# Optimization experiments

Measured on AMD Instinct MI355X. Metric: run time of the kernel, lower is better.

The kernel has to match this reference:

```python
import jax, jax.numpy as jnp
import numpy as np

EMB = 1024
NUM_HEADS = 16


def setup_inputs() -> dict:
    key = jax.random.key(0)
    k_x, k_k, k_q, k_v, k_u, k_b = jax.random.split(key, 6)
    b, s, e = 4, 2048, EMB
    lim = 1.0 / np.sqrt(e)
    return {
        "x": jax.random.normal(k_x, (b, s, e), dtype=jnp.float32),
        "Wk": jax.random.uniform(k_k, (e, e), jnp.float32, -lim, lim),
        "Wq": jax.random.uniform(k_q, (e, e), jnp.float32, -lim, lim),
        "Wv": jax.random.uniform(k_v, (e, e), jnp.float32, -lim, lim),
        "Wu": jax.random.uniform(k_u, (e, e), jnp.float32, -lim, lim),
        "bu": jax.random.uniform(k_b, (e,), jnp.float32, -lim, lim),
    }


def reference(x, Wk, Wq, Wv, Wu, bu):
    b, s, e = x.shape
    h = NUM_HEADS
    d = e // h
    # scale q and k each by emb**(-1/4), as in the original (note: emb, not head_size)
    scale = e ** -0.25
    # project and split heads: (b, h, s, d)
    q = (x @ Wq.T).reshape(b, s, h, d).transpose(0, 2, 1, 3) * scale
    k = (x @ Wk.T).reshape(b, s, h, d).transpose(0, 2, 1, 3) * scale
    v = (x @ Wv.T).reshape(b, s, h, d).transpose(0, 2, 1, 3)
    # attention scores (b, h, s, s)
    dot = jnp.einsum("bhqd,bhkd->bhqk", q, k)
    # causal mask: strictly-upper triangle (offset=1) set to -inf
    causal = jnp.triu(jnp.ones((s, s), dtype=bool), k=1)
    dot = jnp.where(causal[None, None, :, :], -jnp.inf, dot)
    attn = jax.nn.softmax(dot, axis=-1)
    out = jnp.einsum("bhqk,bhkd->bhqd", attn, v)
    out = out.transpose(0, 2, 1, 3).reshape(b, s, e)
    return out @ Wu.T + bu
```

## Files before the change

kernel.cpp:

```cpp
#include <hip/hip_runtime.h>
#include <stdint.h>
#include <math.h>


typedef __attribute__((ext_vector_type(8))) short bf16x8;
typedef __attribute__((ext_vector_type(4))) float f32x4;
typedef __attribute__((ext_vector_type(16))) float f32x16;
typedef __attribute__((ext_vector_type(4))) int i32x4;
typedef __attribute__((ext_vector_type(4))) short s16x4;

#define GLOAD_LDS16(gp, lp)                                                     \
  __builtin_amdgcn_global_load_lds(                                             \
      (__attribute__((address_space(1))) void*)(gp),                            \
      (__attribute__((address_space(3))) void*)(lp), 16, 0, 0)

__device__ __forceinline__ short f2bf(float f) {
  union { float f; uint32_t u; } v; v.f = f;
  uint32_t r = v.u + 0x7FFFu + ((v.u >> 16) & 1u);
  return (short)(r >> 16);
}
__device__ __forceinline__ float bf2f(short s) {
  union { uint32_t u; float f; } v; v.u = ((uint32_t)(uint16_t)s) << 16;
  return v.f;
}
__device__ __forceinline__ short f2bfn(float f) {
  union { __bf16 h; short s; } u; u.h = (__bf16)f; return u.s;
}
__device__ __forceinline__ uint32_t pk2n(float a, float b) {
  union { __bf16 h[2]; uint32_t u; } v;
  v.h[0] = (__bf16)a; v.h[1] = (__bf16)b;
  return v.u;
}

__device__ __forceinline__ void swap32(uint32_t a, uint32_t b, int hi,
                                       uint32_t& out0, uint32_t& out1) {
#if __has_builtin(__builtin_amdgcn_permlane32_swap)
  typedef __attribute__((ext_vector_type(2))) int i32x2;
  i32x2 r = __builtin_amdgcn_permlane32_swap((int)a, (int)b, false, false);
  out0 = (uint32_t)r.x; out1 = (uint32_t)r.y;
#else
  uint32_t ta = (uint32_t)__shfl_xor((int)a, 32);
  uint32_t tb = (uint32_t)__shfl_xor((int)b, 32);
  out0 = hi ? tb : a;
  out1 = hi ? b : ta;
#endif
}

__global__ __launch_bounds__(256) void cast_kernel(const float* __restrict__ src,
                                                   short* __restrict__ dst, int n) {
  int i = (blockIdx.x * 256 + threadIdx.x) * 8;
  if (i >= n) return;
  const float4* s = (const float4*)(src + i);
  float4 f0 = s[0], f1 = s[1];
  bf16x8 o;
  o[0] = f2bf(f0.x); o[1] = f2bf(f0.y); o[2] = f2bf(f0.z); o[3] = f2bf(f0.w);
  o[4] = f2bf(f1.x); o[5] = f2bf(f1.y); o[6] = f2bf(f1.z); o[7] = f2bf(f1.w);
  *(bf16x8*)(dst + i) = o;
}

__global__ __launch_bounds__(256) void cast4_kernel(const float* __restrict__ w0,
                                                    const float* __restrict__ w1,
                                                    const float* __restrict__ w2,
                                                    const float* __restrict__ w3,
                                                    short* o0, short* o1, short* o2, short* o3) {
  const float* src = (blockIdx.y == 0) ? w0 : (blockIdx.y == 1) ? w1 : (blockIdx.y == 2) ? w2 : w3;
  short* dst = (blockIdx.y == 0) ? o0 : (blockIdx.y == 1) ? o1 : (blockIdx.y == 2) ? o2 : o3;
  int i = (blockIdx.x * 256 + threadIdx.x) * 8;
  const float4* s = (const float4*)(src + i);
  float4 f0 = s[0], f1 = s[1];
  bf16x8 o;
  o[0] = f2bf(f0.x); o[1] = f2bf(f0.y); o[2] = f2bf(f0.z); o[3] = f2bf(f0.w);
  o[4] = f2bf(f1.x); o[5] = f2bf(f1.y); o[6] = f2bf(f1.z); o[7] = f2bf(f1.w);
  *(bf16x8*)(dst + i) = o;
}

template <bool F32OUT>
__device__ __forceinline__ void gemm_bt_core(const short* __restrict__ A,
                                             const short* __restrict__ Bm,
                                             short* __restrict__ Cb,
                                             float* __restrict__ Cf,
                                             const float* __restrict__ bias) {
  __shared__ short a_lds[128 * 64];
  __shared__ short b_lds[128 * 64];
  const int tid = threadIdx.x;
  const int w = tid >> 6, l = tid & 63;
  const int l15 = l & 15, lhi = l >> 4;
  const int wr = w >> 1, wc = w & 1;
  const int row0 = blockIdx.x * 128;
  const int col0 = blockIdx.y * 128;

  f32x4 acc[4][4];
#pragma unroll
  for (int m = 0; m < 4; ++m)
#pragma unroll
    for (int n = 0; n < 4; ++n)
      acc[m][n] = (f32x4){0.f, 0.f, 0.f, 0.f};

  const int o0 = tid * 16;
  const int sr = o0 >> 7;
  const int sc = o0 & 127;

  for (int kt = 0; kt < 16; ++kt) {
    const char* Ab = (const char*)A + (size_t)(row0 + sr) * 2048 + kt * 128 + sc;
    const char* Bb = (const char*)Bm + (size_t)(col0 + sr) * 2048 + kt * 128 + sc;
#pragma unroll
    for (int i = 0; i < 4; ++i) {
      GLOAD_LDS16(Ab + (size_t)i * 32 * 2048, (char*)a_lds + i * 4096 + o0);
      GLOAD_LDS16(Bb + (size_t)i * 32 * 2048, (char*)b_lds + i * 4096 + o0);
    }
    __syncthreads();
#pragma unroll
    for (int kk = 0; kk < 2; ++kk) {
      bf16x8 af[4], bg[4];
#pragma unroll
      for (int m = 0; m < 4; ++m) {
        int r = wr * 64 + m * 16 + l15;
        af[m] = *(const bf16x8*)((const char*)a_lds + r * 128 + kk * 64 + lhi * 16);
      }
#pragma unroll
      for (int n = 0; n < 4; ++n) {
        int r = wc * 64 + n * 16 + l15;
        bg[n] = *(const bf16x8*)((const char*)b_lds + r * 128 + kk * 64 + lhi * 16);
      }
#pragma unroll
      for (int m = 0; m < 4; ++m)
#pragma unroll
        for (int n = 0; n < 4; ++n)
          acc[m][n] = __builtin_amdgcn_mfma_f32_16x16x32_bf16(af[m], bg[n], acc[m][n], 0, 0, 0);
    }
    __syncthreads();
  }

#pragma unroll
  for (int m = 0; m < 4; ++m) {
#pragma unroll
    for (int n = 0; n < 4; ++n) {
      int colg = col0 + wc * 64 + n * 16 + l15;
#pragma unroll
      for (int r = 0; r < 4; ++r) {
        int rowg = row0 + wr * 64 + m * 16 + lhi * 4 + r;
        float v = acc[m][n][r];
        if constexpr (F32OUT) {
          Cf[(size_t)rowg * 1024 + colg] = v + bias[colg];
        } else {
          Cb[(size_t)rowg * 1024 + colg] = f2bfn(v);
        }
      }
    }
  }
}

__global__ __launch_bounds__(256) void gemm_qkv_kernel(const short* __restrict__ xb,
                                                       const short* __restrict__ wq,
                                                       const short* __restrict__ wk,
                                                       const short* __restrict__ wv,
                                                       short* qo, short* ko, short* vo) {
  const short* Bm = (blockIdx.z == 0) ? wq : (blockIdx.z == 1) ? wk : wv;
  short* C = (blockIdx.z == 0) ? qo : (blockIdx.z == 1) ? ko : vo;
  gemm_bt_core<false>(xb, Bm, C, nullptr, nullptr);
}

__global__ __launch_bounds__(256) void gemm_out_kernel(const short* __restrict__ ob,
                                                       const short* __restrict__ wu,
                                                       const float* __restrict__ bias,
                                                       float* __restrict__ out) {
  gemm_bt_core<true>(ob, wu, nullptr, out, bias);
}

__global__ __launch_bounds__(256) void transpose_v_kernel(const short* __restrict__ vb,
                                                          short* __restrict__ vt) {
  int st = blockIdx.x, bh = blockIdx.y;
  int b = bh >> 4, h = bh & 15;
  __shared__ short tile[64][66];
  int tid = threadIdx.x;
  int sl = tid >> 2;
  int d0 = (tid & 3) * 16;
  const short* src = vb + (size_t)(b * 2048 + st * 64 + sl) * 1024 + h * 64 + d0;
  bf16x8 v0 = *(const bf16x8*)(src);
  bf16x8 v1 = *(const bf16x8*)(src + 8);
#pragma unroll
  for (int i = 0; i < 8; ++i) tile[d0 + i][sl] = v0[i];
#pragma unroll
  for (int i = 0; i < 8; ++i) tile[d0 + 8 + i][sl] = v1[i];
  __syncthreads();
  int d = tid >> 2;
  int s0 = (tid & 3) * 16;
  bf16x8 o0, o1;
#pragma unroll
  for (int i = 0; i < 8; ++i) o0[i] = tile[d][s0 + i];
#pragma unroll
  for (int i = 0; i < 8; ++i) o1[i] = tile[d][s0 + 8 + i];
  short* dst = vt + (size_t)(bh * 64 + d) * 2048 + st * 64 + s0;
  *(bf16x8*)dst = o0;
  *(bf16x8*)(dst + 8) = o1;
}

__global__ __launch_bounds__(512) void attn_kernel(const short* __restrict__ qb,
                                                   const short* __restrict__ kb,
                                                   const short* __restrict__ vt,
                                                   short* __restrict__ ob) {
  const float QSCALE = 0.03125f * 1.44269504f;
  const float THR = 11.5416f;
  int id = blockIdx.x;
  int T = 7 - (id >> 6);
  int bh = id & 63;
  int b = bh >> 4, h = bh & 15;
  int wid = threadIdx.x >> 6, l = threadIdx.x & 63;
  int l31 = l & 31, hi = l >> 5;
  int Q0 = T * 256;
  int nk = 4 * (T + 1);
  int qrow0 = Q0 + wid * 32;
  int qg = qrow0 + l31;
  int qmax = qrow0 + 31;

  __shared__ short kv_lds[2][2][64 * 64];

  int tid = threadIdx.x;
  int o = tid * 16;
  int sr = o >> 7;
  int sc0 = (o & 127) ^ ((sr & 7) << 4);
  const short* Ksrc0 = kb + ((size_t)b * 2048 + sr) * 1024 + h * 64 + (sc0 >> 1);
  const short* Vsrc0 = vt + ((size_t)bh * 64 + sr) * 2048 + (sc0 >> 1);

  const short* qbase = qb + ((size_t)(b * 2048 + qg)) * 1024 + h * 64 + hi * 8;
  bf16x8 aq[4];
#pragma unroll
  for (int s = 0; s < 4; ++s) {
    bf16x8 t = *(const bf16x8*)(qbase + s * 16);
#pragma unroll
    for (int j = 0; j < 8; ++j) t[j] = f2bfn(bf2f(t[j]) * QSCALE);
    aq[s] = t;
  }

  f32x16 o_lo = {}, o_hi = {};
  float mr = -INFINITY, lsum = 0.f;

  GLOAD_LDS16(Ksrc0, (char*)&kv_lds[0][0][0] + o);
  GLOAD_LDS16(Vsrc0, (char*)&kv_lds[0][1][0] + o);
  __syncthreads();

  const int swz = (l31 & 7) << 4;
  for (int kt = 0; kt < nk; ++kt) {
    int k0 = kt * 64;
    int cur = kt & 1;
    if (kt + 1 < nk) {
      GLOAD_LDS16(Ksrc0 + (size_t)(k0 + 64) * 1024, (char*)&kv_lds[cur ^ 1][0][0] + o);
      GLOAD_LDS16(Vsrc0 + (k0 + 64), (char*)&kv_lds[cur ^ 1][1][0] + o);
    }
    if (k0 <= qmax) {
      const char* kbase = (const char*)&kv_lds[cur][0][0];
      const char* vbase = (const char*)&kv_lds[cur][1][0];
      f32x16 st0 = {}, st1 = {};
      {
        int rb = l31 * 128;
#pragma unroll
        for (int s = 0; s < 4; ++s) {
          bf16x8 ak = *(const bf16x8*)(kbase + rb + ((s * 32 + hi * 16) ^ swz));
          st0 = __builtin_amdgcn_mfma_f32_32x32x16_bf16(ak, aq[s], st0, 0, 0, 0);
        }
        rb = (l31 + 32) * 128;
#pragma unroll
        for (int s = 0; s < 4; ++s) {
          bf16x8 ak = *(const bf16x8*)(kbase + rb + ((s * 32 + hi * 16) ^ swz));
          st1 = __builtin_amdgcn_mfma_f32_32x32x16_bf16(ak, aq[s], st1, 0, 0, 0);
        }
      }

      if (k0 + 31 > qrow0) {
#pragma unroll
        for (int r = 0; r < 16; ++r) {
          int kk = k0 + (r & 3) + 8 * (r >> 2) + 4 * hi;
          if (kk > qg) st0[r] = -INFINITY;
        }
      }
      if (k0 + 63 > qrow0) {
#pragma unroll
        for (int r = 0; r < 16; ++r) {
          int kk = k0 + 32 + (r & 3) + 8 * (r >> 2) + 4 * hi;
          if (kk > qg) st1[r] = -INFINITY;
        }
      }

      float mx[16];
#pragma unroll
      for (int r = 0; r < 16; ++r) mx[r] = fmaxf(st0[r], st1[r]);
#pragma unroll
      for (int r = 0; r < 8; ++r) mx[r] = fmaxf(mx[r], mx[r + 8]);
#pragma unroll
      for (int r = 0; r < 4; ++r) mx[r] = fmaxf(mx[r], mx[r + 4]);
      float pmax = fmaxf(fmaxf(mx[0], mx[1]), fmaxf(mx[2], mx[3]));
      pmax = fmaxf(pmax, __shfl_xor(pmax, 32));

      if (pmax > mr + THR) {
        float alpha = exp2f(mr - pmax);
        mr = pmax;
        lsum *= alpha;
#pragma unroll
        for (int r = 0; r < 16; ++r) { o_lo[r] *= alpha; o_hi[r] *= alpha; }
      }

#pragma unroll
      for (int r = 0; r < 16; ++r) st0[r] = exp2f(st0[r] - mr);
#pragma unroll
      for (int r = 0; r < 16; ++r) st1[r] = exp2f(st1[r] - mr);
      float sm[16];
#pragma unroll
      for (int r = 0; r < 16; ++r) sm[r] = st0[r] + st1[r];
#pragma unroll
      for (int r = 0; r < 8; ++r) sm[r] += sm[r + 8];
#pragma unroll
      for (int r = 0; r < 4; ++r) sm[r] += sm[r + 4];
      lsum += (sm[0] + sm[1]) + (sm[2] + sm[3]);

      uint32_t a0, a2, b1, b3, c0, c2, d1, d3;
      swap32(pk2n(st0[0], st0[1]),   pk2n(st0[4], st0[5]),   hi, a0, a2);
      swap32(pk2n(st0[2], st0[3]),   pk2n(st0[6], st0[7]),   hi, b1, b3);
      swap32(pk2n(st0[8], st0[9]),   pk2n(st0[12], st0[13]), hi, c0, c2);
      swap32(pk2n(st0[10], st0[11]), pk2n(st0[14], st0[15]), hi, d1, d3);
      i32x4 u0 = {(int)a0, (int)b1, (int)a2, (int)b3};
      i32x4 u1 = {(int)c0, (int)d1, (int)c2, (int)d3};
      swap32(pk2n(st1[0], st1[1]),   pk2n(st1[4], st1[5]),   hi, a0, a2);
      swap32(pk2n(st1[2], st1[3]),   pk2n(st1[6], st1[7]),   hi, b1, b3);
      swap32(pk2n(st1[8], st1[9]),   pk2n(st1[12], st1[13]), hi, c0, c2);
      swap32(pk2n(st1[10], st1[11]), pk2n(st1[14], st1[15]), hi, d1, d3);
      i32x4 u2 = {(int)a0, (int)b1, (int)a2, (int)b3};
      i32x4 u3 = {(int)c0, (int)d1, (int)c2, (int)d3};
      bf16x8 pa0 = __builtin_bit_cast(bf16x8, u0);
      bf16x8 pa1 = __builtin_bit_cast(bf16x8, u1);
      bf16x8 pa2 = __builtin_bit_cast(bf16x8, u2);
      bf16x8 pa3 = __builtin_bit_cast(bf16x8, u3);

      int rlo = l31 * 128, rhi = (l31 + 32) * 128;
      bf16x8 av;
      av = *(const bf16x8*)(vbase + rlo + ((hi * 16) ^ swz));
      o_lo = __builtin_amdgcn_mfma_f32_32x32x16_bf16(av, pa0, o_lo, 0, 0, 0);
      av = *(const bf16x8*)(vbase + rhi + ((hi * 16) ^ swz));
      o_hi = __builtin_amdgcn_mfma_f32_32x32x16_bf16(av, pa0, o_hi, 0, 0, 0);
      av = *(const bf16x8*)(vbase + rlo + ((32 + hi * 16) ^ swz));
      o_lo = __builtin_amdgcn_mfma_f32_32x32x16_bf16(av, pa1, o_lo, 0, 0, 0);
      av = *(const bf16x8*)(vbase + rhi + ((32 + hi * 16) ^ swz));
      o_hi = __builtin_amdgcn_mfma_f32_32x32x16_bf16(av, pa1, o_hi, 0, 0, 0);
      av = *(const bf16x8*)(vbase + rlo + ((64 + hi * 16) ^ swz));
      o_lo = __builtin_amdgcn_mfma_f32_32x32x16_bf16(av, pa2, o_lo, 0, 0, 0);
      av = *(const bf16x8*)(vbase + rhi + ((64 + hi * 16) ^ swz));
      o_hi = __builtin_amdgcn_mfma_f32_32x32x16_bf16(av, pa2, o_hi, 0, 0, 0);
      av = *(const bf16x8*)(vbase + rlo + ((96 + hi * 16) ^ swz));
      o_lo = __builtin_amdgcn_mfma_f32_32x32x16_bf16(av, pa3, o_lo, 0, 0, 0);
      av = *(const bf16x8*)(vbase + rhi + ((96 + hi * 16) ^ swz));
      o_hi = __builtin_amdgcn_mfma_f32_32x32x16_bf16(av, pa3, o_hi, 0, 0, 0);
    }
    __syncthreads();
  }

  lsum += __shfl_xor(lsum, 32);
  float inv = 1.0f / lsum;
  short* obase = ob + (size_t)(b * 2048 + qg) * 1024 + h * 64;
#pragma unroll
  for (int g = 0; g < 4; ++g) {
    int d0 = 8 * g + 4 * hi;
    s16x4 v0, v1;
#pragma unroll
    for (int j = 0; j < 4; ++j) {
      v0[j] = f2bfn(o_lo[4 * g + j] * inv);
      v1[j] = f2bfn(o_hi[4 * g + j] * inv);
    }
    *(s16x4*)(obase + d0) = v0;
    *(s16x4*)(obase + 32 + d0) = v1;
  }
}

extern "C" void kernel_launch(void* const* d_in, const int* in_sizes, int n_in,
                              void* d_out, int out_size, void* d_ws, size_t ws_size,
                              hipStream_t stream) {
  const float* x  = (const float*)d_in[0];
  const float* Wk = (const float*)d_in[1];
  const float* Wq = (const float*)d_in[2];
  const float* Wv = (const float*)d_in[3];
  const float* Wu = (const float*)d_in[4];
  const float* bu = (const float*)d_in[5];
  float* out = (float*)d_out;

  char* ws = (char*)d_ws;
  const size_t MB = 1u << 20;
  short* xb  = (short*)(ws + 0 * MB);
  short* qb  = (short*)(ws + 16 * MB);
  short* kb  = (short*)(ws + 32 * MB);
  short* vb  = (short*)(ws + 48 * MB);
  short* vtb = (short*)(ws + 64 * MB);
  short* ob  = (short*)(ws + 80 * MB);
  short* wqb = (short*)(ws + 96 * MB);
  short* wkb = (short*)(ws + 98 * MB);
  short* wvb = (short*)(ws + 100 * MB);
  short* wub = (short*)(ws + 102 * MB);

  cast_kernel<<<4096, 256, 0, stream>>>(x, xb, 8388608);
  cast4_kernel<<<dim3(512, 4), 256, 0, stream>>>(Wq, Wk, Wv, Wu, wqb, wkb, wvb, wub);

  gemm_qkv_kernel<<<dim3(64, 8, 3), 256, 0, stream>>>(xb, wqb, wkb, wvb, qb, kb, vb);
  transpose_v_kernel<<<dim3(32, 64), 256, 0, stream>>>(vb, vtb);
  attn_kernel<<<512, 512, 0, stream>>>(qb, kb, vtb, ob);
  gemm_out_kernel<<<dim3(64, 8), 256, 0, stream>>>(ob, wub, bu, out);
}
```

Measured before the change: 193.9 us.

## Pre-permute Q/K/V into MFMA fragment layout and pair causal tiles per block

Replaces the V transpose with two kernels that rewrite Q, K and V into MFMA fragment order, so attention loads come in as contiguous, conflict-free 16-byte lanes without swizzling. The attention kernel shrinks to 256 threads per block. Each block processes two complementary causal query tiles (j and 15-j) to even out work across blocks. K/V staging becomes a two-deep prefetch with explicit vmcnt waits and raw barriers. The cost is an extra launch, a full extra pass over Q/K/V memory, and workspace buffers that alias earlier ones.

```diff
diff --git a/kernel.cpp b/kernel.cpp
--- a/kernel.cpp
+++ b/kernel.cpp
@@ -13,6 +13,8 @@
   __builtin_amdgcn_global_load_lds(                                             \
       (__attribute__((address_space(1))) void*)(gp),                            \
       (__attribute__((address_space(3))) void*)(lp), 16, 0, 0)
+
+#define WAITVM(N) asm volatile("s_waitcnt vmcnt(" #N ")" ::: "memory")
 
 __device__ __forceinline__ short f2bf(float f) {
   union { float f; uint32_t u; } v; v.f = f;
@@ -167,206 +169,234 @@
   gemm_bt_core<true>(ob, wu, nullptr, out, bias);
 }
 
-__global__ __launch_bounds__(256) void transpose_v_kernel(const short* __restrict__ vb,
-                                                          short* __restrict__ vt) {
-  int st = blockIdx.x, bh = blockIdx.y;
+__global__ __launch_bounds__(256) void frag_qk_kernel(const short* __restrict__ qb,
+                                                      const short* __restrict__ kb,
+                                                      short* __restrict__ qf,
+                                                      short* __restrict__ kf) {
+  int t = blockIdx.x, bh = blockIdx.y;
   int b = bh >> 4, h = bh & 15;
-  __shared__ short tile[64][66];
+  __shared__ short q_t[32][72], k_t[32][72];
   int tid = threadIdx.x;
-  int sl = tid >> 2;
-  int d0 = (tid & 3) * 16;
-  const short* src = vb + (size_t)(b * 2048 + st * 64 + sl) * 1024 + h * 64 + d0;
-  bf16x8 v0 = *(const bf16x8*)(src);
-  bf16x8 v1 = *(const bf16x8*)(src + 8);
-#pragma unroll
-  for (int i = 0; i < 8; ++i) tile[d0 + i][sl] = v0[i];
-#pragma unroll
-  for (int i = 0; i < 8; ++i) tile[d0 + 8 + i][sl] = v1[i];
+  int row = tid >> 3, seg = tid & 7;
+  size_t src = ((size_t)(b * 2048 + t * 32 + row)) * 1024 + h * 64 + seg * 8;
+  *(bf16x8*)&q_t[row][seg * 8] = *(const bf16x8*)(qb + src);
+  *(bf16x8*)&k_t[row][seg * 8] = *(const bf16x8*)(kb + src);
   __syncthreads();
-  int d = tid >> 2;
-  int s0 = (tid & 3) * 16;
-  bf16x8 o0, o1;
-#pragma unroll
-  for (int i = 0; i < 8; ++i) o0[i] = tile[d][s0 + i];
-#pragma unroll
-  for (int i = 0; i < 8; ++i) o1[i] = tile[d][s0 + 8 + i];
-  short* dst = vt + (size_t)(bh * 64 + d) * 2048 + st * 64 + s0;
-  *(bf16x8*)dst = o0;
-  *(bf16x8*)(dst + 8) = o1;
-}
-
-__global__ __launch_bounds__(512) void attn_kernel(const short* __restrict__ qb,
-                                                   const short* __restrict__ kb,
-                                                   const short* __restrict__ vt,
+  int s = tid >> 6, l = tid & 63, l31 = l & 31, hi = l >> 5;
+  bf16x8 cq = *(const bf16x8*)&q_t[l31][hi * 8 + s * 16];
+  bf16x8 ck = *(const bf16x8*)&k_t[l31][hi * 8 + s * 16];
+  size_t dst = ((size_t)bh * 64 + t) * 2048 + s * 512 + l * 8;
+  *(bf16x8*)(qf + dst) = cq;
+  *(bf16x8*)(kf + dst) = ck;
+}
+
+__global__ __launch_bounds__(256) void frag_v_kernel(const short* __restrict__ vb,
+                                                     short* __restrict__ vf) {
+  int t = blockIdx.x, bh = blockIdx.y;
+  int b = bh >> 4, h = bh & 15;
+  __shared__ short v_t[32][72];
+  int tid = threadIdx.x;
+  int row = tid >> 3, seg = tid & 7;
+  *(bf16x8*)&v_t[row][seg * 8] =
+      *(const bf16x8*)(vb + ((size_t)(b * 2048 + t * 32 + row)) * 1024 + h * 64 + seg * 8);
+  __syncthreads();
+  int u = tid >> 6, l = tid & 63, l31 = l & 31, hi = l >> 5;
+  int dblk = u >> 1, koff = u & 1;
+  bf16x8 c;
+#pragma unroll
+  for (int j = 0; j < 8; ++j) c[j] = v_t[koff * 16 + hi * 8 + j][dblk * 32 + l31];
+  *(bf16x8*)(vf + ((size_t)bh * 64 + t) * 2048 + u * 512 + l * 8) = c;
+}
+
+__global__ __launch_bounds__(256) void attn_kernel(const short* __restrict__ qf,
+                                                   const short* __restrict__ kf,
+                                                   const short* __restrict__ vf,
                                                    short* __restrict__ ob) {
   const float QSCALE = 0.03125f * 1.44269504f;
   const float THR = 11.5416f;
   int id = blockIdx.x;
-  int T = 7 - (id >> 6);
+  int p = id >> 6;
   int bh = id & 63;
   int b = bh >> 4, h = bh & 15;
   int wid = threadIdx.x >> 6, l = threadIdx.x & 63;
   int l31 = l & 31, hi = l >> 5;
-  int Q0 = T * 256;
-  int nk = 4 * (T + 1);
-  int qrow0 = Q0 + wid * 32;
-  int qg = qrow0 + l31;
-  int qmax = qrow0 + 31;
-
-  __shared__ short kv_lds[2][2][64 * 64];
-
   int tid = threadIdx.x;
-  int o = tid * 16;
-  int sr = o >> 7;
-  int sc0 = (o & 127) ^ ((sr & 7) << 4);
-  const short* Ksrc0 = kb + ((size_t)b * 2048 + sr) * 1024 + h * 64 + (sc0 >> 1);
-  const short* Vsrc0 = vt + ((size_t)bh * 64 + sr) * 2048 + (sc0 >> 1);
-
-  const short* qbase = qb + ((size_t)(b * 2048 + qg)) * 1024 + h * 64 + hi * 8;
-  bf16x8 aq[4];
-#pragma unroll
-  for (int s = 0; s < 4; ++s) {
-    bf16x8 t = *(const bf16x8*)(qbase + s * 16);
-#pragma unroll
-    for (int j = 0; j < 8; ++j) t[j] = f2bfn(bf2f(t[j]) * QSCALE);
-    aq[s] = t;
+
+  __shared__ short kbuf[2][4096];
+  __shared__ short vbuf[2][4096];
+
+  const short* qfb = qf + (size_t)bh * 131072;
+  const short* kfb = kf + (size_t)bh * 131072;
+  const short* vfb = vf + (size_t)bh * 131072;
+
+#define STAGE(t, bi) do {                                                  \
+    const short* ks_ = kfb + (t) * 4096 + tid * 8;                         \
+    const short* vs_ = vfb + (t) * 4096 + tid * 8;                         \
+    GLOAD_LDS16(ks_,        (char*)&kbuf[bi][0] + tid * 16);               \
+    GLOAD_LDS16(ks_ + 2048, (char*)&kbuf[bi][0] + 4096 + tid * 16);        \
+    GLOAD_LDS16(vs_,        (char*)&vbuf[bi][0] + tid * 16);               \
+    GLOAD_LDS16(vs_ + 2048, (char*)&vbuf[bi][0] + 4096 + tid * 16);        \
+  } while (0)
+
+#pragma unroll
+  for (int part = 0; part < 2; ++part) {
+    int j = part ? (15 - p) : p;
+    int qt = 4 * j + wid;
+    int qrow0 = qt * 32;
+    int qg = qrow0 + l31;
+    int qmax = qrow0 + 31;
+    int nk = 2 * (j + 1);
+
+    bf16x8 aq[4];
+    {
+      const short* qp = qfb + qt * 2048 + l * 8;
+#pragma unroll
+      for (int s = 0; s < 4; ++s) {
+        bf16x8 t = *(const bf16x8*)(qp + s * 512);
+#pragma unroll
+        for (int jj = 0; jj < 8; ++jj) t[jj] = f2bfn(bf2f(t[jj]) * QSCALE);
+        aq[s] = t;
+      }
+    }
+
+    f32x16 o_lo = {}, o_hi = {};
+    float mr = -INFINITY, lsum = 0.f;
+
+    STAGE(0, 0);
+    STAGE(1, 1);
+    WAITVM(4);
+    __builtin_amdgcn_s_barrier();
+    __builtin_amdgcn_sched_barrier(0);
+
+    for (int t = 0; t < nk; ++t) {
+      int k0 = t * 64;
+      int cur = t & 1;
+      if (k0 <= qmax) {
+        const char* kb_ = (const char*)&kbuf[cur][0];
+        const char* vb_ = (const char*)&vbuf[cur][0];
+        f32x16 st0 = {}, st1 = {};
+#pragma unroll
+        for (int s = 0; s < 4; ++s) {
+          bf16x8 ak = *(const bf16x8*)(kb_ + (s * 64 + l) * 16);
+          st0 = __builtin_amdgcn_mfma_f32_32x32x16_bf16(ak, aq[s], st0, 0, 0, 0);
+        }
+#pragma unroll
+        for (int s = 0; s < 4; ++s) {
+          bf16x8 ak = *(const bf16x8*)(kb_ + 4096 + (s * 64 + l) * 16);
+          st1 = __builtin_amdgcn_mfma_f32_32x32x16_bf16(ak, aq[s], st1, 0, 0, 0);
+        }
+
+        if (k0 + 31 > qrow0) {
+#pragma unroll
+          for (int r = 0; r < 16; ++r) {
+            int kk = k0 + (r & 3) + 8 * (r >> 2) + 4 * hi;
+            if (kk > qg) st0[r] = -INFINITY;
+          }
+        }
+        if (k0 + 63 > qrow0) {
+#pragma unroll
+          for (int r = 0; r < 16; ++r) {
+            int kk = k0 + 32 + (r & 3) + 8 * (r >> 2) + 4 * hi;
+            if (kk > qg) st1[r] = -INFINITY;
+          }
+        }
+
+        float mx[16];
+#pragma unroll
+        for (int r = 0; r < 16; ++r) mx[r] = fmaxf(st0[r], st1[r]);
+#pragma unroll
+        for (int r = 0; r < 8; ++r) mx[r] = fmaxf(mx[r], mx[r + 8]);
+#pragma unroll
+        for (int r = 0; r < 4; ++r) mx[r] = fmaxf(mx[r], mx[r + 4]);
+        float pmax = fmaxf(fmaxf(mx[0], mx[1]), fmaxf(mx[2], mx[3]));
+        pmax = fmaxf(pmax, __shfl_xor(pmax, 32));
+
+        if (pmax > mr + THR) {
+          float alpha = exp2f(mr - pmax);
+          mr = pmax;
+          lsum *= alpha;
+#pragma unroll
+          for (int r = 0; r < 16; ++r) { o_lo[r] *= alpha; o_hi[r] *= alpha; }
+        }
+
+#pragma unroll
+        for (int r = 0; r < 16; ++r) st0[r] = exp2f(st0[r] - mr);
+#pragma unroll
+        for (int r = 0; r < 16; ++r) st1[r] = exp2f(st1[r] - mr);
+        float sm[16];
+#pragma unroll
+        for (int r = 0; r < 16; ++r) sm[r] = st0[r] + st1[r];
+#pragma unroll
+        for (int r = 0; r < 8; ++r) sm[r] += sm[r + 8];
+#pragma unroll
+        for (int r = 0; r < 4; ++r) sm[r] += sm[r + 4];
+        lsum += (sm[0] + sm[1]) + (sm[2] + sm[3]);
+
+        uint32_t a0, a2, b1, b3, c0, c2, d1, d3;
+        swap32(pk2n(st0[0], st0[1]),   pk2n(st0[4], st0[5]),   hi, a0, a2);
+        swap32(pk2n(st0[2], st0[3]),   pk2n(st0[6], st0[7]),   hi, b1, b3);
+        swap32(pk2n(st0[8], st0[9]),   pk2n(st0[12], st0[13]), hi, c0, c2);
+        swap32(pk2n(st0[10], st0[11]), pk2n(st0[14], st0[15]), hi, d1, d3);
+        i32x4 u0 = {(int)a0, (int)b1, (int)a2, (int)b3};
+        i32x4 u1 = {(int)c0, (int)d1, (int)c2, (int)d3};
+        swap32(pk2n(st1[0], st1[1]),   pk2n(st1[4], st1[5]),   hi, a0, a2);
+        swap32(pk2n(st1[2], st1[3]),   pk2n(st1[6], st1[7]),   hi, b1, b3);
+        swap32(pk2n(st1[8], st1[9]),   pk2n(st1[12], st1[13]), hi, c0, c2);
+        swap32(pk2n(st1[10], st1[11]), pk2n(st1[14], st1[15]), hi, d1, d3);
+        i32x4 u2 = {(int)a0, (int)b1, (int)a2, (int)b3};
+        i32x4 u3 = {(int)c0, (int)d1, (int)c2, (int)d3};
+        bf16x8 pa0 = __builtin_bit_cast(bf16x8, u0);
+        bf16x8 pa1 = __builtin_bit_cast(bf16x8, u1);
+        bf16x8 pa2 = __builtin_bit_cast(bf16x8, u2);
+        bf16x8 pa3 = __builtin_bit_cast(bf16x8, u3);
+
+        bf16x8 av;
+        av = *(const bf16x8*)(vb_ + (0 * 64 + l) * 16);
+        o_lo = __builtin_amdgcn_mfma_f32_32x32x16_bf16(av, pa0, o_lo, 0, 0, 0);
+        av = *(const bf16x8*)(vb_ + (1 * 64 + l) * 16);
+        o_lo = __builtin_amdgcn_mfma_f32_32x32x16_bf16(av, pa1, o_lo, 0, 0, 0);
+        av = *(const bf16x8*)(vb_ + 4096 + (0 * 64 + l) * 16);
+        o_lo = __builtin_amdgcn_mfma_f32_32x32x16_bf16(av, pa2, o_lo, 0, 0, 0);
+        av = *(const bf16x8*)(vb_ + 4096 + (1 * 64 + l) * 16);
+        o_lo = __builtin_amdgcn_mfma_f32_32x32x16_bf16(av, pa3, o_lo, 0, 0, 0);
+        av = *(const bf16x8*)(vb_ + (2 * 64 + l) * 16);
+        o_hi = __builtin_amdgcn_mfma_f32_32x32x16_bf16(av, pa0, o_hi, 0, 0, 0);
+        av = *(const bf16x8*)(vb_ + (3 * 64 + l) * 16);
+        o_hi = __builtin_amdgcn_mfma_f32_32x32x16_bf16(av, pa1, o_hi, 0, 0, 0);
+        av = *(const bf16x8*)(vb_ + 4096 + (2 * 64 + l) * 16);
+        o_hi = __builtin_amdgcn_mfma_f32_32x32x16_bf16(av, pa2, o_hi, 0, 0, 0);
+        av = *(const bf16x8*)(vb_ + 4096 + (3 * 64 + l) * 16);
+        o_hi = __builtin_amdgcn_mfma_f32_32x32x16_bf16(av, pa3, o_hi, 0, 0, 0);
+      }
+      __builtin_amdgcn_s_barrier();
+      __builtin_amdgcn_sched_barrier(0);
+      if (t + 2 < nk) {
+        STAGE(t + 2, cur);
+        WAITVM(4);
+      } else {
+        WAITVM(0);
+      }
+      __builtin_amdgcn_s_barrier();
+      __builtin_amdgcn_sched_barrier(0);
+    }
+
+    lsum += __shfl_xor(lsum, 32);
+    float inv = 1.0f / lsum;
+    short* obase = ob + (size_t)(b * 2048 + qg) * 1024 + h * 64;
+#pragma unroll
+    for (int g = 0; g < 4; ++g) {
+      int d0 = 8 * g + 4 * hi;
+      s16x4 v0, v1;
+#pragma unroll
+      for (int jj = 0; jj < 4; ++jj) {
+        v0[jj] = f2bfn(o_lo[4 * g + jj] * inv);
+        v1[jj] = f2bfn(o_hi[4 * g + jj] * inv);
+      }
+      *(s16x4*)(obase + d0) = v0;
+      *(s16x4*)(obase + 32 + d0) = v1;
+    }
   }
-
-  f32x16 o_lo = {}, o_hi = {};
-  float mr = -INFINITY, lsum = 0.f;
-
-  GLOAD_LDS16(Ksrc0, (char*)&kv_lds[0][0][0] + o);
-  GLOAD_LDS16(Vsrc0, (char*)&kv_lds[0][1][0] + o);
-  __syncthreads();
-
-  const int swz = (l31 & 7) << 4;
-  for (int kt = 0; kt < nk; ++kt) {
-    int k0 = kt * 64;
-    int cur = kt & 1;
-    if (kt + 1 < nk) {
-      GLOAD_LDS16(Ksrc0 + (size_t)(k0 + 64) * 1024, (char*)&kv_lds[cur ^ 1][0][0] + o);
-      GLOAD_LDS16(Vsrc0 + (k0 + 64), (char*)&kv_lds[cur ^ 1][1][0] + o);
-    }
-    if (k0 <= qmax) {
-      const char* kbase = (const char*)&kv_lds[cur][0][0];
-      const char* vbase = (const char*)&kv_lds[cur][1][0];
-      f32x16 st0 = {}, st1 = {};
-      {
-        int rb = l31 * 128;
-#pragma unroll
-        for (int s = 0; s < 4; ++s) {
-          bf16x8 ak = *(const bf16x8*)(kbase + rb + ((s * 32 + hi * 16) ^ swz));
-          st0 = __builtin_amdgcn_mfma_f32_32x32x16_bf16(ak, aq[s], st0, 0, 0, 0);
-        }
-        rb = (l31 + 32) * 128;
-#pragma unroll
-        for (int s = 0; s < 4; ++s) {
-          bf16x8 ak = *(const bf16x8*)(kbase + rb + ((s * 32 + hi * 16) ^ swz));
-          st1 = __builtin_amdgcn_mfma_f32_32x32x16_bf16(ak, aq[s], st1, 0, 0, 0);
-        }
-      }
-
-      if (k0 + 31 > qrow0) {
-#pragma unroll
-        for (int r = 0; r < 16; ++r) {
-          int kk = k0 + (r & 3) + 8 * (r >> 2) + 4 * hi;
-          if (kk > qg) st0[r] = -INFINITY;
-        }
-      }
-      if (k0 + 63 > qrow0) {
-#pragma unroll
-        for (int r = 0; r < 16; ++r) {
-          int kk = k0 + 32 + (r & 3) + 8 * (r >> 2) + 4 * hi;
-          if (kk > qg) st1[r] = -INFINITY;
-        }
-      }
-
-      float mx[16];
-#pragma unroll
-      for (int r = 0; r < 16; ++r) mx[r] = fmaxf(st0[r], st1[r]);
-#pragma unroll
-      for (int r = 0; r < 8; ++r) mx[r] = fmaxf(mx[r], mx[r + 8]);
-#pragma unroll
-      for (int r = 0; r < 4; ++r) mx[r] = fmaxf(mx[r], mx[r + 4]);
-      float pmax = fmaxf(fmaxf(mx[0], mx[1]), fmaxf(mx[2], mx[3]));
-      pmax = fmaxf(pmax, __shfl_xor(pmax, 32));
-
-      if (pmax > mr + THR) {
-        float alpha = exp2f(mr - pmax);
-        mr = pmax;
-        lsum *= alpha;
-#pragma unroll
-        for (int r = 0; r < 16; ++r) { o_lo[r] *= alpha; o_hi[r] *= alpha; }
-      }
-
-#pragma unroll
-      for (int r = 0; r < 16; ++r) st0[r] = exp2f(st0[r] - mr);
-#pragma unroll
-      for (int r = 0; r < 16; ++r) st1[r] = exp2f(st1[r] - mr);
-      float sm[16];
-#pragma unroll
-      for (int r = 0; r < 16; ++r) sm[r] = st0[r] + st1[r];
-#pragma unroll
-      for (int r = 0; r < 8; ++r) sm[r] += sm[r + 8];
-#pragma unroll
-      for (int r = 0; r < 4; ++r) sm[r] += sm[r + 4];
-      lsum += (sm[0] + sm[1]) + (sm[2] + sm[3]);
-
-      uint32_t a0, a2, b1, b3, c0, c2, d1, d3;
-      swap32(pk2n(st0[0], st0[1]),   pk2n(st0[4], st0[5]),   hi, a0, a2);
-      swap32(pk2n(st0[2], st0[3]),   pk2n(st0[6], st0[7]),   hi, b1, b3);
-      swap32(pk2n(st0[8], st0[9]),   pk2n(st0[12], st0[13]), hi, c0, c2);
-      swap32(pk2n(st0[10], st0[11]), pk2n(st0[14], st0[15]), hi, d1, d3);
-      i32x4 u0 = {(int)a0, (int)b1, (int)a2, (int)b3};
-      i32x4 u1 = {(int)c0, (int)d1, (int)c2, (int)d3};
-      swap32(pk2n(st1[0], st1[1]),   pk2n(st1[4], st1[5]),   hi, a0, a2);
-      swap32(pk2n(st1[2], st1[3]),   pk2n(st1[6], st1[7]),   hi, b1, b3);
-      swap32(pk2n(st1[8], st1[9]),   pk2n(st1[12], st1[13]), hi, c0, c2);
-      swap32(pk2n(st1[10], st1[11]), pk2n(st1[14], st1[15]), hi, d1, d3);
-      i32x4 u2 = {(int)a0, (int)b1, (int)a2, (int)b3};
-      i32x4 u3 = {(int)c0, (int)d1, (int)c2, (int)d3};
-      bf16x8 pa0 = __builtin_bit_cast(bf16x8, u0);
-      bf16x8 pa1 = __builtin_bit_cast(bf16x8, u1);
-      bf16x8 pa2 = __builtin_bit_cast(bf16x8, u2);
-      bf16x8 pa3 = __builtin_bit_cast(bf16x8, u3);
-
-      int rlo = l31 * 128, rhi = (l31 + 32) * 128;
-      bf16x8 av;
-      av = *(const bf16x8*)(vbase + rlo + ((hi * 16) ^ swz));
-      o_lo = __builtin_amdgcn_mfma_f32_32x32x16_bf16(av, pa0, o_lo, 0, 0, 0);
-      av = *(const bf16x8*)(vbase + rhi + ((hi * 16) ^ swz));
-      o_hi = __builtin_amdgcn_mfma_f32_32x32x16_bf16(av, pa0, o_hi, 0, 0, 0);
-      av = *(const bf16x8*)(vbase + rlo + ((32 + hi * 16) ^ swz));
-      o_lo = __builtin_amdgcn_mfma_f32_32x32x16_bf16(av, pa1, o_lo, 0, 0, 0);
-      av = *(const bf16x8*)(vbase + rhi + ((32 + hi * 16) ^ swz));
-      o_hi = __builtin_amdgcn_mfma_f32_32x32x16_bf16(av, pa1, o_hi, 0, 0, 0);
-      av = *(const bf16x8*)(vbase + rlo + ((64 + hi * 16) ^ swz));
-      o_lo = __builtin_amdgcn_mfma_f32_32x32x16_bf16(av, pa2, o_lo, 0, 0, 0);
-      av = *(const bf16x8*)(vbase + rhi + ((64 + hi * 16) ^ swz));
-      o_hi = __builtin_amdgcn_mfma_f32_32x32x16_bf16(av, pa2, o_hi, 0, 0, 0);
-      av = *(const bf16x8*)(vbase + rlo + ((96 + hi * 16) ^ swz));
-      o_lo = __builtin_amdgcn_mfma_f32_32x32x16_bf16(av, pa3, o_lo, 0, 0, 0);
-      av = *(const bf16x8*)(vbase + rhi + ((96 + hi * 16) ^ swz));
-      o_hi = __builtin_amdgcn_mfma_f32_32x32x16_bf16(av, pa3, o_hi, 0, 0, 0);
-    }
-    __syncthreads();
-  }
-
-  lsum += __shfl_xor(lsum, 32);
-  float inv = 1.0f / lsum;
-  short* obase = ob + (size_t)(b * 2048 + qg) * 1024 + h * 64;
-#pragma unroll
-  for (int g = 0; g < 4; ++g) {
-    int d0 = 8 * g + 4 * hi;
-    s16x4 v0, v1;
-#pragma unroll
-    for (int j = 0; j < 4; ++j) {
-      v0[j] = f2bfn(o_lo[4 * g + j] * inv);
-      v1[j] = f2bfn(o_hi[4 * g + j] * inv);
-    }
-    *(s16x4*)(obase + d0) = v0;
-    *(s16x4*)(obase + 32 + d0) = v1;
-  }
+#undef STAGE
 }
 
 extern "C" void kernel_launch(void* const* d_in, const int* in_sizes, int n_in,
@@ -383,10 +413,12 @@
   char* ws = (char*)d_ws;
   const size_t MB = 1u << 20;
   short* xb  = (short*)(ws + 0 * MB);
+  short* qf  = (short*)(ws + 0 * MB);
   short* qb  = (short*)(ws + 16 * MB);
+  short* vfb = (short*)(ws + 16 * MB);
   short* kb  = (short*)(ws + 32 * MB);
   short* vb  = (short*)(ws + 48 * MB);
-  short* vtb = (short*)(ws + 64 * MB);
+  short* kfb = (short*)(ws + 64 * MB);
   short* ob  = (short*)(ws + 80 * MB);
   short* wqb = (short*)(ws + 96 * MB);
   short* wkb = (short*)(ws + 98 * MB);
@@ -397,7 +429,8 @@
   cast4_kernel<<<dim3(512, 4), 256, 0, stream>>>(Wq, Wk, Wv, Wu, wqb, wkb, wvb, wub);
 
   gemm_qkv_kernel<<<dim3(64, 8, 3), 256, 0, stream>>>(xb, wqb, wkb, wvb, qb, kb, vb);
-  transpose_v_kernel<<<dim3(32, 64), 256, 0, stream>>>(vb, vtb);
-  attn_kernel<<<512, 512, 0, stream>>>(qb, kb, vtb, ob);
+  frag_qk_kernel<<<dim3(64, 64), 256, 0, stream>>>(qb, kb, qf, kfb);
+  frag_v_kernel<<<dim3(64, 64), 256, 0, stream>>>(vb, vfb);
+  attn_kernel<<<512, 256, 0, stream>>>(qf, kfb, vfb, ob);
   gemm_out_kernel<<<dim3(64, 8), 256, 0, stream>>>(ob, wub, bu, out);
 }
```

Result: slower. 211.3 us (+9.0%).
